# Kernel tuning notes

Hardware: AMD Instinct MI355X
Metric: run time of the kernel (lower is better)

The kernel has to match this reference:

```python
import jax, jax.numpy as jnp
import numpy as np

N, E, DIN, H, L, NCLS = 50000, 800000, 256, 384, 6, 2
EPS = 1e-5

def setup_inputs() -> dict:
    key = jax.random.key(0)
    ks = jax.random.split(key, 24)
    def lin(k, fan_in, shape):
        b = 1.0 / np.sqrt(fan_in)
        return jax.random.uniform(k, shape, jnp.float32, -b, b)
    inp = {}
    inp['x'] = jax.random.normal(ks[0], (N, DIN), jnp.float32)
    inp['edge_index'] = jax.random.randint(ks[1], (2, E), 0, N, jnp.int32)
    inp['W_in'] = lin(ks[2], DIN, (DIN, H)); inp['b_in'] = lin(ks[3], DIN, (H,))
    inp['bn0_g'] = jnp.ones((H,), jnp.float32); inp['bn0_b'] = jnp.zeros((H,), jnp.float32)
    inp['Wl'] = lin(ks[4], H, (L, H, H)); inp['bl'] = lin(ks[5], H, (L, H))
    inp['Wr'] = lin(ks[6], H, (L, H, H))
    inp['bn_g'] = jnp.ones((L, H), jnp.float32); inp['bn_b'] = jnp.zeros((L, H), jnp.float32)
    inp['Wskip'] = lin(ks[7], H, (L // 2, H, H)); inp['bskip'] = lin(ks[8], H, (L // 2, H))
    inp['W1'] = lin(ks[9], H, (H, H // 2)); inp['b1'] = lin(ks[10], H, (H // 2,))
    inp['W2'] = lin(ks[11], H // 2, (H // 2, H // 4)); inp['b2'] = lin(ks[12], H // 2, (H // 4,))
    inp['W3'] = lin(ks[13], H // 4, (H // 4, NCLS)); inp['b3'] = lin(ks[14], H // 4, (NCLS,))
    return inp

def _batchnorm(h, g, b):
    mu = jnp.mean(h, axis=0)
    var = jnp.mean(jnp.square(h - mu), axis=0)  # biased, as torch BN training
    return (h - mu) * jax.lax.rsqrt(var + EPS) * g + b

def reference(x, edge_index, W_in, b_in, bn0_g, bn0_b, Wl, bl, Wr, bn_g, bn_b,
              Wskip, bskip, W1, b1, W2, b2, W3, b3):
    row, col = edge_index[0], edge_index[1]  # messages flow row -> col
    cnt = jax.ops.segment_sum(jnp.ones((E,), jnp.float32), col, num_segments=N)
    inv_cnt = (1.0 / jnp.maximum(cnt, 1.0))[:, None]  # [N,1]

    h = _batchnorm(x @ W_in + b_in, bn0_g, bn0_b)
    h = jax.nn.relu(h)  # dropout is identity in eval

    skip_idx = 0
    for i in range(L):
        identity = h
        agg = jax.ops.segment_sum(h[row], col, num_segments=N) * inv_cnt  # mean aggregation
        h = agg @ Wl[i] + bl[i] + h @ Wr[i]  # SAGEConv: lin_l(mean) + lin_r(x)
        h = jax.nn.relu(_batchnorm(h, bn_g[i], bn_b[i]))
        if (i + 1) % 2 == 0 and skip_idx < L // 2:
            h = h + identity @ Wskip[skip_idx] + bskip[skip_idx]
            skip_idx += 1

    embeddings = h
    h = jax.nn.relu(h @ W1 + b1)
    h = jax.nn.relu(h @ W2 + b2)
    out = h @ W3 + b3
    return (out, embeddings)
```

## Files before the change

kernel.cpp:

```cpp
#include <hip/hip_runtime.h>

#define H 384
#define EPS 1e-5f

typedef __attribute__((ext_vector_type(8))) short bf8v;
typedef __attribute__((ext_vector_type(8))) unsigned short us8;
typedef __attribute__((ext_vector_type(4))) float f32x4;

__device__ __forceinline__ float b2f(unsigned short b) {
    return __builtin_bit_cast(float, (unsigned)b << 16);
}
__device__ __forceinline__ unsigned short f2b(float f) {
    unsigned u = __builtin_bit_cast(unsigned, f);
    u += 0x7FFFu + ((u >> 16) & 1u);
    return (unsigned short)(u >> 16);
}

__global__ __launch_bounds__(256) void gemm_mfma(
    const unsigned short* __restrict__ A1, const unsigned short* __restrict__ W1t,
    const unsigned short* __restrict__ A2, const unsigned short* __restrict__ W2t,
    const float* __restrict__ bias, unsigned short* __restrict__ Cb,
    float* __restrict__ bnsum, float* __restrict__ bnsq,
    int Nr, int K, int M, int relu)
{
    __shared__ unsigned short As[128][40];
    __shared__ unsigned short Bs[128][40];
    __shared__ float s_stat[256];
    const int t = threadIdx.x;
    const int wave = t >> 6, lane = t & 63;
    const int wr = (wave >> 1) * 64, wc = (wave & 1) * 64;
    const int r0 = blockIdx.x * 128, c0 = blockIdx.y * 128;
    const int lm = lane & 15, lq = lane >> 4;
    f32x4 acc[4][4] = {};

    const int npass = (A2 != nullptr) ? 2 : 1;
    for (int pass = 0; pass < npass; ++pass) {
        const unsigned short* __restrict__ A = pass ? A2 : A1;
        const unsigned short* __restrict__ W = pass ? W2t : W1t;
        for (int k0 = 0; k0 < K; k0 += 32) {
            #pragma unroll
            for (int q = 0; q < 2; ++q) {
                int c = t + q * 256;
                int r = c >> 2, ko = (c & 3) * 8;
                int gr = r0 + r; if (gr >= Nr) gr = Nr - 1;
                *(bf8v*)&As[r][ko] = *(const bf8v*)(A + (long)gr * K + k0 + ko);
            }
            #pragma unroll
            for (int q = 0; q < 2; ++q) {
                int c = t + q * 256;
                int r = c >> 2, ko = (c & 3) * 8;
                int gc = c0 + r; if (gc >= M) gc = M - 1;
                *(bf8v*)&Bs[r][ko] = *(const bf8v*)(W + (long)gc * K + k0 + ko);
            }
            __syncthreads();
            bf8v af[4], bf[4];
            #pragma unroll
            for (int i = 0; i < 4; ++i)
                af[i] = *(const bf8v*)&As[wr + i * 16 + lm][lq * 8];
            #pragma unroll
            for (int j = 0; j < 4; ++j)
                bf[j] = *(const bf8v*)&Bs[wc + j * 16 + lm][lq * 8];
            #pragma unroll
            for (int i = 0; i < 4; ++i)
                #pragma unroll
                for (int j = 0; j < 4; ++j)
                    acc[i][j] = __builtin_amdgcn_mfma_f32_16x16x32_bf16(
                        af[i], bf[j], acc[i][j], 0, 0, 0);
            __syncthreads();
        }
    }

    const bool do_stats = (bnsum != nullptr);
    if (do_stats) {
        s_stat[t] = 0.f;
        __syncthreads();
    }

    #pragma unroll
    for (int j = 0; j < 4; ++j) {
        int lcol = wc + j * 16 + lm;
        int col = c0 + lcol;
        if (col >= M) continue;
        float bi = bias[col];
        float ls = 0.f, lss = 0.f;
        #pragma unroll
        for (int i = 0; i < 4; ++i) {
            #pragma unroll
            for (int r = 0; r < 4; ++r) {
                int rowi = r0 + wr + i * 16 + lq * 4 + r;
                if (rowi >= Nr) continue;
                float v = acc[i][j][r] + bi;
                ls += v; lss += v * v;
                float vo = relu ? fmaxf(v, 0.f) : v;
                Cb[(long)rowi * M + col] = f2b(vo);
            }
        }
        if (do_stats) {
            atomicAdd(&s_stat[lcol], ls);
            atomicAdd(&s_stat[128 + lcol], lss);
        }
    }
    if (do_stats) {
        __syncthreads();
        if (t < 128) {
            int col = c0 + t;
            if (col < M) {
                atomicAdd(&bnsum[col], s_stat[t]);
                atomicAdd(&bnsq[col], s_stat[128 + t]);
            }
        }
    }
}

__global__ void wt_convert(const float* __restrict__ W, unsigned short* __restrict__ Wt,
                           int total, int K, int M)
{
    int idx = blockIdx.x * 256 + threadIdx.x;
    if (idx >= total) return;
    int l = idx / (K * M), rem = idx - l * K * M;
    int k = rem / M, m = rem - k * M;
    Wt[(long)l * K * M + (long)m * K + k] = f2b(W[idx]);
}

__global__ void f2b_vec(const float* __restrict__ X, unsigned short* __restrict__ Y, int n4)
{
    int idx = blockIdx.x * 256 + threadIdx.x;
    if (idx >= n4) return;
    float4 v = *(const float4*)(X + idx * 4);
    ushort4 o = {f2b(v.x), f2b(v.y), f2b(v.z), f2b(v.w)};
    *(ushort4*)(Y + idx * 4) = o;
}

__global__ void count_edges_i(const int* __restrict__ col, int* __restrict__ cnt, int E)
{
    int e = blockIdx.x * 256 + threadIdx.x;
    if (e < E) atomicAdd(&cnt[col[e]], 1);
}

__global__ __launch_bounds__(1024) void exscan_csr(const int* __restrict__ cnt,
                                                   int* __restrict__ offs, int n)
{
    __shared__ int s[1024];
    const int t = threadIdx.x;
    const int chunk = (n + 1023) >> 10;
    int lo = t * chunk, hi = lo + chunk;
    if (lo > n) lo = n;
    if (hi > n) hi = n;
    int sum = 0;
    for (int i = lo; i < hi; ++i) sum += cnt[i];
    s[t] = sum;
    __syncthreads();
    for (int d = 1; d < 1024; d <<= 1) {
        int o = (t >= d) ? s[t - d] : 0;
        __syncthreads();
        s[t] += o;
        __syncthreads();
    }
    int base = (t == 0) ? 0 : s[t - 1];
    for (int i = lo; i < hi; ++i) { offs[i] = base; base += cnt[i]; }
    if (t == 1023) offs[n] = s[1023];
}

__global__ void fill_csr(const int* __restrict__ row, const int* __restrict__ col,
                         const int* __restrict__ offs, int* __restrict__ cursor,
                         int* __restrict__ csr_rows, int E)
{
    int e = blockIdx.x * 256 + threadIdx.x;
    if (e < E) {
        int c = col[e];
        int p = offs[c] + atomicAdd(&cursor[c], 1);
        csr_rows[p] = row[e];
    }
}

__global__ void inv_from_cnt(const int* __restrict__ cnt, float* __restrict__ inv, int n)
{
    int i = blockIdx.x * 256 + threadIdx.x;
    if (i < n) inv[i] = 1.0f / fmaxf((float)cnt[i], 1.0f);
}

__global__ __launch_bounds__(384) void agg_gather(
    const unsigned short* __restrict__ hb, const int* __restrict__ csr_rows,
    const int* __restrict__ offs, const float* __restrict__ inv,
    unsigned short* __restrict__ aggb, int N)
{
    int g = threadIdx.x / 48;
    int lane = threadIdx.x - g * 48;
    int node = blockIdx.x * 8 + g;
    if (node >= N) return;
    const int lo = offs[node], hi = offs[node + 1];
    float s[8] = {};
    int e = lo;
    for (; e + 3 < hi; e += 4) {
        int r0 = csr_rows[e], r1 = csr_rows[e + 1];
        int r2 = csr_rows[e + 2], r3 = csr_rows[e + 3];
        us8 v0 = *(const us8*)(hb + (long)r0 * H + lane * 8);
        us8 v1 = *(const us8*)(hb + (long)r1 * H + lane * 8);
        us8 v2 = *(const us8*)(hb + (long)r2 * H + lane * 8);
        us8 v3 = *(const us8*)(hb + (long)r3 * H + lane * 8);
        #pragma unroll
        for (int q = 0; q < 8; ++q)
            s[q] += (b2f(v0[q]) + b2f(v1[q])) + (b2f(v2[q]) + b2f(v3[q]));
    }
    for (; e < hi; ++e) {
        us8 v = *(const us8*)(hb + (long)csr_rows[e] * H + lane * 8);
        #pragma unroll
        for (int q = 0; q < 8; ++q) s[q] += b2f(v[q]);
    }
    float sc = inv[node];
    us8 o;
    #pragma unroll
    for (int q = 0; q < 8; ++q) o[q] = f2b(s[q] * sc);
    *(us8*)(aggb + (long)node * H + lane * 8) = o;
}

__global__ __launch_bounds__(256) void bn_apply(
    const unsigned short* __restrict__ X, const float* __restrict__ bnsum,
    const float* __restrict__ bnsq, const float* __restrict__ g,
    const float* __restrict__ b, const unsigned short* __restrict__ S,
    unsigned short* __restrict__ outb, float* __restrict__ outf,
    int Nr, int total4)
{
    __shared__ float sc[H], sh[H];
    const int t = threadIdx.x;
    for (int j = t; j < H; j += 256) {
        float mu  = bnsum[j] / (float)Nr;
        float var = bnsq[j] / (float)Nr - mu * mu;
        float s   = g[j] * rsqrtf(fmaxf(var, 0.f) + EPS);
        sc[j] = s;
        sh[j] = b[j] - mu * s;
    }
    __syncthreads();
    int idx = blockIdx.x * 256 + t;
    if (idx >= total4) return;
    int base = idx * 4;
    int j = base % H;
    ushort4 v = *(const ushort4*)(X + base);
    float o0 = fmaxf(b2f(v.x) * sc[j + 0] + sh[j + 0], 0.f);
    float o1 = fmaxf(b2f(v.y) * sc[j + 1] + sh[j + 1], 0.f);
    float o2 = fmaxf(b2f(v.z) * sc[j + 2] + sh[j + 2], 0.f);
    float o3 = fmaxf(b2f(v.w) * sc[j + 3] + sh[j + 3], 0.f);
    if (S) {
        ushort4 s4 = *(const ushort4*)(S + base);
        o0 += b2f(s4.x); o1 += b2f(s4.y); o2 += b2f(s4.z); o3 += b2f(s4.w);
    }
    ushort4 o = {f2b(o0), f2b(o1), f2b(o2), f2b(o3)};
    *(ushort4*)(outb + base) = o;
    if (outf) {
        float4 of = {o0, o1, o2, o3};
        *(float4*)(outf + base) = of;
    }
}

__global__ void mlp3(const unsigned short* __restrict__ m2, const float* __restrict__ W3,
                     const float* __restrict__ b3, float* __restrict__ out, int N)
{
    int n = blockIdx.x * 256 + threadIdx.x;
    if (n >= N) return;
    float a0 = b3[0], a1 = b3[1];
    const unsigned short* r = m2 + (long)n * 96;
    #pragma unroll 4
    for (int k = 0; k < 96; ++k) {
        float v = b2f(r[k]);
        a0 += v * W3[k * 2];
        a1 += v * W3[k * 2 + 1];
    }
    out[n * 2 + 0] = a0;
    out[n * 2 + 1] = a1;
}

extern "C" void kernel_launch(void* const* d_in, const int* in_sizes, int n_in,
                              void* d_out, int out_size, void* d_ws, size_t ws_size,
                              hipStream_t stream)
{
    const float* x     = (const float*)d_in[0];
    const int*   ei    = (const int*)d_in[1];
    const float* W_in  = (const float*)d_in[2];
    const float* b_in  = (const float*)d_in[3];
    const float* bn0_g = (const float*)d_in[4];
    const float* bn0_b = (const float*)d_in[5];
    const float* Wl    = (const float*)d_in[6];
    const float* bl    = (const float*)d_in[7];
    const float* Wr    = (const float*)d_in[8];
    const float* bn_g  = (const float*)d_in[9];
    const float* bn_b  = (const float*)d_in[10];
    const float* Wskip = (const float*)d_in[11];
    const float* bskip = (const float*)d_in[12];
    const float* W1    = (const float*)d_in[13];
    const float* b1    = (const float*)d_in[14];
    const float* W2    = (const float*)d_in[15];
    const float* b2    = (const float*)d_in[16];
    const float* W3    = (const float*)d_in[17];
    const float* b3    = (const float*)d_in[18];

    const int DIN = 256;
    const int N = in_sizes[0] / DIN;
    const int E = in_sizes[1] / 2;
    const int* row = ei;
    const int* col = ei + E;
    const long NH = (long)N * H;

    unsigned short* tmp      = (unsigned short*)d_ws;
    unsigned short* hb       = tmp + NH;
    unsigned short* aggb     = hb + NH;
    unsigned short* Sbuf     = aggb + NH;
    unsigned short* xb       = Sbuf + NH;
    float*          inv      = (float*)(xb + (long)N * DIN);
    int*            offs     = (int*)(inv + N);
    int*            csr_rows = offs + (N + 1);
    int*            cnt      = csr_rows + E;
    int*            cursor   = cnt + N;
    float*          stats    = (float*)(cursor + N);
    unsigned short* Wint     = (unsigned short*)(stats + 14 * H);
    unsigned short* Wlt      = Wint + (long)H * DIN;
    unsigned short* Wrt      = Wlt + 6L * H * H;
    unsigned short* Wskipt   = Wrt + 6L * H * H;
    unsigned short* W1t      = Wskipt + 3L * H * H;
    unsigned short* W2t      = W1t + 192L * H;
    float* out = (float*)d_out;
    float* emb = out + (long)N * 2;

    dim3 blk(256);
    const int rg128 = (N + 127) / 128;
    const int app_grid = (int)((NH / 4 + 255) / 256);

    hipMemsetAsync(cnt, 0, (2L * N + 14 * H) * sizeof(float), stream);

    count_edges_i<<<(E + 255) / 256, blk, 0, stream>>>(col, cnt, E);
    exscan_csr<<<1, 1024, 0, stream>>>(cnt, offs, N);
    inv_from_cnt<<<(N + 255) / 256, blk, 0, stream>>>(cnt, inv, N);
    fill_csr<<<(E + 255) / 256, blk, 0, stream>>>(row, col, offs, cursor, csr_rows, E);

    {
        int n1 = H * DIN;
        wt_convert<<<(n1 + 255) / 256, blk, 0, stream>>>(W_in, Wint, n1, DIN, H);
        int n2 = 6 * H * H;
        wt_convert<<<(n2 + 255) / 256, blk, 0, stream>>>(Wl, Wlt, n2, H, H);
        wt_convert<<<(n2 + 255) / 256, blk, 0, stream>>>(Wr, Wrt, n2, H, H);
        int n3 = 3 * H * H;
        wt_convert<<<(n3 + 255) / 256, blk, 0, stream>>>(Wskip, Wskipt, n3, H, H);
        int n4 = H * 192;
        wt_convert<<<(n4 + 255) / 256, blk, 0, stream>>>(W1, W1t, n4, H, 192);
        int n5 = 192 * 96;
        wt_convert<<<(n5 + 255) / 256, blk, 0, stream>>>(W2, W2t, n5, 192, 96);
    }

    {
        int n4 = N * DIN / 4;
        f2b_vec<<<(n4 + 255) / 256, blk, 0, stream>>>(x, xb, n4);
    }
    gemm_mfma<<<dim3(rg128, 3), blk, 0, stream>>>(
        xb, Wint, nullptr, nullptr, b_in, tmp, stats, stats + H, N, DIN, H, 0);
    bn_apply<<<app_grid, blk, 0, stream>>>(
        tmp, stats, stats + H, bn0_g, bn0_b, nullptr, hb, nullptr, N, (int)(NH / 4));

    int skip_idx = 0;
    for (int i = 0; i < 6; ++i) {
        float* bs = stats + (i + 1) * 2 * H;
        agg_gather<<<(N + 7) / 8, 384, 0, stream>>>(hb, csr_rows, offs, inv, aggb, N);

        gemm_mfma<<<dim3(rg128, 3), blk, 0, stream>>>(
            aggb, Wlt + (long)i * H * H, hb, Wrt + (long)i * H * H,
            bl + i * H, tmp, bs, bs + H, N, H, H, 0);

        const unsigned short* S = nullptr;
        if ((i & 1) == 1) {
            gemm_mfma<<<dim3(rg128, 3), blk, 0, stream>>>(
                hb, Wskipt + (long)skip_idx * H * H, nullptr, nullptr,
                bskip + skip_idx * H, Sbuf, nullptr, nullptr, N, H, H, 0);
            skip_idx++;
            S = Sbuf;
        }
        bn_apply<<<app_grid, blk, 0, stream>>>(
            tmp, bs, bs + H, bn_g + i * H, bn_b + i * H, S, hb,
            (i == 5) ? emb : nullptr, N, (int)(NH / 4));
    }

    unsigned short* m1b = aggb;
    unsigned short* m2b = tmp;
    gemm_mfma<<<dim3(rg128, 2), blk, 0, stream>>>(
        hb, W1t, nullptr, nullptr, b1, m1b, nullptr, nullptr, N, H, 192, 1);
    gemm_mfma<<<dim3(rg128, 1), blk, 0, stream>>>(
        m1b, W2t, nullptr, nullptr, b2, m2b, nullptr, nullptr, N, 192, 96, 1);
    mlp3<<<(N + 255) / 256, blk, 0, stream>>>(m2b, W3, b3, out, N);
}
```

Before: 1.856 ms.

## Use direct global-to-LDS loads, XOR swizzle, K=64 tiles and staged vector stores in GEMM

The GEMM now loads A and W tiles straight into LDS with global_load_lds, using an XOR-swizzled layout that avoids bank conflicts. It doubles the K step to 64, so there are half as many barriers per tile. The epilogue stages the bf16 output through LDS and writes 16-byte vector stores instead of scattered 2-byte stores. The grid is transposed so blocks sharing the same row tile run next to each other, which helps L2 reuse of the A rows. The trade-offs are more LDS use and an extra epilogue barrier, and the 17408-element smem buffer must also cover the padded C staging area.

Result: slower. 4.216 ms (+127.2%).

```diff
diff --git a/kernel.cpp b/kernel.cpp
--- a/kernel.cpp
+++ b/kernel.cpp
@@ -14,6 +14,12 @@
     unsigned u = __builtin_bit_cast(unsigned, f);
     u += 0x7FFFu + ((u >> 16) & 1u);
     return (unsigned short)(u >> 16);
+}
+
+__device__ __forceinline__ void gload16(const unsigned short* g, unsigned short* l) {
+    __builtin_amdgcn_global_load_lds(
+        (const __attribute__((address_space(1))) void*)g,
+        (__attribute__((address_space(3))) void*)l, 16, 0, 0);
 }
 
 __global__ __launch_bounds__(256) void gemm_mfma(
@@ -23,92 +29,101 @@
     float* __restrict__ bnsum, float* __restrict__ bnsq,
     int Nr, int K, int M, int relu)
 {
-    __shared__ unsigned short As[128][40];
-    __shared__ unsigned short Bs[128][40];
+    __shared__ unsigned short smem[17408];
     __shared__ float s_stat[256];
+    unsigned short* sA = smem;
+    unsigned short* sB = smem + 8192;
     const int t = threadIdx.x;
     const int wave = t >> 6, lane = t & 63;
     const int wr = (wave >> 1) * 64, wc = (wave & 1) * 64;
-    const int r0 = blockIdx.x * 128, c0 = blockIdx.y * 128;
+    const int c0 = blockIdx.x * 128, r0 = blockIdx.y * 128;
     const int lm = lane & 15, lq = lane >> 4;
+    const int l8 = lane >> 3;
+    const int gsw8 = ((lane & 7) ^ l8) * 8;
     f32x4 acc[4][4] = {};
+
+    s_stat[t] = 0.f;
 
     const int npass = (A2 != nullptr) ? 2 : 1;
     for (int pass = 0; pass < npass; ++pass) {
         const unsigned short* __restrict__ A = pass ? A2 : A1;
         const unsigned short* __restrict__ W = pass ? W2t : W1t;
-        for (int k0 = 0; k0 < K; k0 += 32) {
+        for (int k0 = 0; k0 < K; k0 += 64) {
             #pragma unroll
-            for (int q = 0; q < 2; ++q) {
-                int c = t + q * 256;
-                int r = c >> 2, ko = (c & 3) * 8;
-                int gr = r0 + r; if (gr >= Nr) gr = Nr - 1;
-                *(bf8v*)&As[r][ko] = *(const bf8v*)(A + (long)gr * K + k0 + ko);
-            }
-            #pragma unroll
-            for (int q = 0; q < 2; ++q) {
-                int c = t + q * 256;
-                int r = c >> 2, ko = (c & 3) * 8;
-                int gc = c0 + r; if (gc >= M) gc = M - 1;
-                *(bf8v*)&Bs[r][ko] = *(const bf8v*)(W + (long)gc * K + k0 + ko);
+            for (int s = 0; s < 4; ++s) {
+                const int seg = (wave << 2) + s;
+                const int tr = (seg << 3) + l8;
+                int gr = r0 + tr; if (gr >= Nr) gr = Nr - 1;
+                gload16(A + (long)gr * K + k0 + gsw8, sA + (seg << 9));
+                int gc = c0 + tr; if (gc >= M) gc = M - 1;
+                gload16(W + (long)gc * K + k0 + gsw8, sB + (seg << 9));
             }
             __syncthreads();
-            bf8v af[4], bf[4];
             #pragma unroll
-            for (int i = 0; i < 4; ++i)
-                af[i] = *(const bf8v*)&As[wr + i * 16 + lm][lq * 8];
-            #pragma unroll
-            for (int j = 0; j < 4; ++j)
-                bf[j] = *(const bf8v*)&Bs[wc + j * 16 + lm][lq * 8];
-            #pragma unroll
-            for (int i = 0; i < 4; ++i)
+            for (int kk = 0; kk < 2; ++kk) {
+                const int pc = (((kk << 2) | lq) ^ (lm & 7)) << 3;
+                bf8v af[4], bf[4];
                 #pragma unroll
-                for (int j = 0; j < 4; ++j)
-                    acc[i][j] = __builtin_amdgcn_mfma_f32_16x16x32_bf16(
-                        af[i], bf[j], acc[i][j], 0, 0, 0);
+                for (int i = 0; i < 4; ++i) {
+                    const int ra = wr + (i << 4) + lm;
+                    af[i] = *(const bf8v*)(sA + (ra << 6) + pc);
+                    const int rb = wc + (i << 4) + lm;
+                    bf[i] = *(const bf8v*)(sB + (rb << 6) + pc);
+                }
+                #pragma unroll
+                for (int i = 0; i < 4; ++i)
+                    #pragma unroll
+                    for (int j = 0; j < 4; ++j)
+                        acc[i][j] = __builtin_amdgcn_mfma_f32_16x16x32_bf16(
+                            af[i], bf[j], acc[i][j], 0, 0, 0);
+            }
             __syncthreads();
         }
     }
 
     const bool do_stats = (bnsum != nullptr);
-    if (do_stats) {
-        s_stat[t] = 0.f;
-        __syncthreads();
-    }
+    unsigned short* sC = smem;
 
     #pragma unroll
-    for (int j = 0; j < 4; ++j) {
-        int lcol = wc + j * 16 + lm;
-        int col = c0 + lcol;
-        if (col >= M) continue;
-        float bi = bias[col];
+    for (int jj = 0; jj < 4; ++jj) {
+        const int j = (jj + lq) & 3;
+        const int lcol = wc + (j << 4) + lm;
+        const int col = c0 + lcol;
+        const float bi = (col < M) ? bias[col] : 0.f;
         float ls = 0.f, lss = 0.f;
         #pragma unroll
         for (int i = 0; i < 4; ++i) {
+            const int lrow = wr + (i << 4) + (lq << 2);
             #pragma unroll
             for (int r = 0; r < 4; ++r) {
-                int rowi = r0 + wr + i * 16 + lq * 4 + r;
-                if (rowi >= Nr) continue;
                 float v = acc[i][j][r] + bi;
-                ls += v; lss += v * v;
-                float vo = relu ? fmaxf(v, 0.f) : v;
-                Cb[(long)rowi * M + col] = f2b(vo);
+                if (r0 + lrow + r < Nr) { ls += v; lss += v * v; }
+                sC[(lrow + r) * 136 + lcol] = f2b(relu ? fmaxf(v, 0.f) : v);
             }
         }
-        if (do_stats) {
+        if (do_stats && col < M) {
             atomicAdd(&s_stat[lcol], ls);
             atomicAdd(&s_stat[128 + lcol], lss);
         }
     }
-    if (do_stats) {
-        __syncthreads();
-        if (t < 128) {
-            int col = c0 + t;
-            if (col < M) {
-                atomicAdd(&bnsum[col], s_stat[t]);
-                atomicAdd(&bnsq[col], s_stat[128 + t]);
-            }
+    __syncthreads();
+    if (do_stats && t < 128) {
+        int col = c0 + t;
+        if (col < M) {
+            atomicAdd(&bnsum[col], s_stat[t]);
+            atomicAdd(&bnsq[col], s_stat[128 + t]);
         }
+    }
+    #pragma unroll
+    for (int it = 0; it < 8; ++it) {
+        const int idx = (it << 8) + t;
+        const int lrow = idx >> 4;
+        const int ch = idx & 15;
+        const int rowg = r0 + lrow;
+        const int col = c0 + (ch << 3);
+        if (rowg < Nr && col < M)
+            *(bf8v*)(Cb + (long)rowg * M + col) =
+                *(const bf8v*)(sC + lrow * 136 + (ch << 3));
     }
 }
 
@@ -305,18 +320,18 @@
     unsigned short* aggb     = hb + NH;
     unsigned short* Sbuf     = aggb + NH;
     unsigned short* xb       = Sbuf + NH;
-    float*          inv      = (float*)(xb + (long)N * DIN);
+    unsigned short* Wint     = xb + (long)N * DIN;
+    unsigned short* Wlt      = Wint + (long)H * DIN;
+    unsigned short* Wrt      = Wlt + 6L * H * H;
+    unsigned short* Wskipt   = Wrt + 6L * H * H;
+    unsigned short* W1t      = Wskipt + 3L * H * H;
+    unsigned short* W2t      = W1t + 192L * H;
+    float*          inv      = (float*)(W2t + 96L * 192);
     int*            offs     = (int*)(inv + N);
     int*            csr_rows = offs + (N + 1);
     int*            cnt      = csr_rows + E;
     int*            cursor   = cnt + N;
     float*          stats    = (float*)(cursor + N);
-    unsigned short* Wint     = (unsigned short*)(stats + 14 * H);
-    unsigned short* Wlt      = Wint + (long)H * DIN;
-    unsigned short* Wrt      = Wlt + 6L * H * H;
-    unsigned short* Wskipt   = Wrt + 6L * H * H;
-    unsigned short* W1t      = Wskipt + 3L * H * H;
-    unsigned short* W2t      = W1t + 192L * H;
     float* out = (float*)d_out;
     float* emb = out + (long)N * 2;
 
@@ -349,7 +364,7 @@
         int n4 = N * DIN / 4;
         f2b_vec<<<(n4 + 255) / 256, blk, 0, stream>>>(x, xb, n4);
     }
-    gemm_mfma<<<dim3(rg128, 3), blk, 0, stream>>>(
+    gemm_mfma<<<dim3(3, rg128), blk, 0, stream>>>(
         xb, Wint, nullptr, nullptr, b_in, tmp, stats, stats + H, N, DIN, H, 0);
     bn_apply<<<app_grid, blk, 0, stream>>>(
         tmp, stats, stats + H, bn0_g, bn0_b, nullptr, hb, nullptr, N, (int)(NH / 4));
@@ -359,13 +374,13 @@
         float* bs = stats + (i + 1) * 2 * H;
         agg_gather<<<(N + 7) / 8, 384, 0, stream>>>(hb, csr_rows, offs, inv, aggb, N);
 
-        gemm_mfma<<<dim3(rg128, 3), blk, 0, stream>>>(
+        gemm_mfma<<<dim3(3, rg128), blk, 0, stream>>>(
             aggb, Wlt + (long)i * H * H, hb, Wrt + (long)i * H * H,
             bl + i * H, tmp, bs, bs + H, N, H, H, 0);
 
         const unsigned short* S = nullptr;
         if ((i & 1) == 1) {
-            gemm_mfma<<<dim3(rg128, 3), blk, 0, stream>>>(
+            gemm_mfma<<<dim3(3, rg128), blk, 0, stream>>>(
                 hb, Wskipt + (long)skip_idx * H * H, nullptr, nullptr,
                 bskip + skip_idx * H, Sbuf, nullptr, nullptr, N, H, H, 0);
             skip_idx++;
@@ -378,9 +393,9 @@
 
     unsigned short* m1b = aggb;
     unsigned short* m2b = tmp;
-    gemm_mfma<<<dim3(rg128, 2), blk, 0, stream>>>(
+    gemm_mfma<<<dim3(2, rg128), blk, 0, stream>>>(
         hb, W1t, nullptr, nullptr, b1, m1b, nullptr, nullptr, N, H, 192, 1);
-    gemm_mfma<<<dim3(rg128, 1), blk, 0, stream>>>(
+    gemm_mfma<<<dim3(1, rg128), blk, 0, stream>>>(
         m1b, W2t, nullptr, nullptr, b2, m2b, nullptr, nullptr, N, 192, 96, 1);
     mlp3<<<(N + 255) / 256, blk, 0, stream>>>(m2b, W3, b3, out, N);
 }
```
